# Kernel optimization log

Measured on AMD Instinct MI355X. Metric: run time of the kernel, lower is better.

The kernel has to match this reference:

```python
import jax, jax.numpy as jnp
import numpy as np

B, DIM, H, W = 8, 512, 32, 32
NUM_HEADS, KEY_DIM, VALUE_DIM, DIM_OUT = 8, 64, 64, 512


def setup_inputs() -> dict:
    key = jax.random.key(0)
    ks = jax.random.split(key, 5)
    return {
        "x": jax.random.normal(ks[0], (B, DIM, H, W), dtype=jnp.float32),
        "query_proj": jax.random.normal(ks[1], (NUM_HEADS, KEY_DIM, DIM), dtype=jnp.float32),
        "key_proj": jax.random.normal(ks[2], (DIM, KEY_DIM), dtype=jnp.float32),
        "value_proj": jax.random.normal(ks[3], (DIM, VALUE_DIM), dtype=jnp.float32),
        "out_proj": jax.random.normal(ks[4], (DIM_OUT, NUM_HEADS, VALUE_DIM), dtype=jnp.float32),
    }


def reference(x, query_proj, key_proj, value_proj, out_proj):
    b, d, h, w = x.shape
    key_dim = query_proj.shape[1]
    scale = key_dim ** (-0.5)
    # flatten spatial dims to tokens: [b, n, d] where n = h*w (m == x here)
    rx = jnp.transpose(x.reshape(b, d, h * w), (0, 2, 1))
    q = jnp.einsum('bnd,hkd->bnhk', rx, query_proj)
    k = jnp.einsum('bmd,dk->bmk', rx, key_proj)          # single shared K head
    attn = jax.nn.softmax(jnp.einsum('bnhk,bmk->bnhm', q, k) * scale, axis=-1)
    v = jnp.einsum('bmd,dv->bmv', rx, value_proj)        # single shared V head
    o = jnp.einsum('bnhm,bmv->bnhv', attn, v)
    result = jnp.einsum('bnhv,dhv->bdn', o, out_proj)
    return result.reshape(b, -1, h, w)
```

## Files before the change

kernel.cpp:

```cpp
#include <hip/hip_runtime.h>
#include <math.h>

#define BATCH 8
#define DIMD  512
#define NTOK  1024
#define NH    8
#define CQKV  640
#define DOUT  512

typedef __attribute__((ext_vector_type(8))) short short8;
typedef __attribute__((ext_vector_type(4))) short short4v;
typedef __attribute__((ext_vector_type(4))) float f32x4;

__device__ __forceinline__ short bf16rn(float x) {
    unsigned u = __float_as_uint(x);
    u += 0x7FFF + ((u >> 16) & 1);
    return (short)(u >> 16);
}
__device__ __forceinline__ float bf16tof(short s) {
    return __uint_as_float(((unsigned)(unsigned short)s) << 16);
}
struct HL { short h, l; };
__device__ __forceinline__ HL bf16split(float x) {
    HL r;
    r.h = bf16rn(x);
    r.l = bf16rn(x - bf16tof(r.h));
    return r;
}
__device__ __forceinline__ void dma16(const short* g, short* l) {
    __builtin_amdgcn_global_load_lds(
        (const __attribute__((address_space(1))) unsigned int*)g,
        (__attribute__((address_space(3))) unsigned int*)l, 16, 0, 0);
}
__device__ __forceinline__ float swzmax16(float v) {
    v = fmaxf(v, __int_as_float(__builtin_amdgcn_ds_swizzle(__float_as_int(v), 0x041F)));
    v = fmaxf(v, __int_as_float(__builtin_amdgcn_ds_swizzle(__float_as_int(v), 0x081F)));
    v = fmaxf(v, __int_as_float(__builtin_amdgcn_ds_swizzle(__float_as_int(v), 0x101F)));
    v = fmaxf(v, __int_as_float(__builtin_amdgcn_ds_swizzle(__float_as_int(v), 0x201F)));
    return v;
}
__device__ __forceinline__ unsigned packbf2(float f0, float f1) {
    return __builtin_amdgcn_perm(__float_as_uint(f1), __float_as_uint(f0), 0x07060302);
}


__global__ __launch_bounds__(256) void prepack_all(const float* __restrict__ x,
                                                   const float* __restrict__ qp,
                                                   const float* __restrict__ kp,
                                                   const float* __restrict__ vp,
                                                   const float* __restrict__ wout,
                                                   short* __restrict__ whi,
                                                   short* __restrict__ wlo,
                                                   short* __restrict__ xhi,
                                                   short* __restrict__ xlo,
                                                   short* __restrict__ wof) {
    __shared__ float Cs[64][65];
    const int blk = blockIdx.x;
    const int t = threadIdx.x;
    if (blk < 1024) {
        const int nt = blk & 15, dt = (blk >> 4) & 7, b = blk >> 7;
        #pragma unroll
        for (int i = 0; i < 4; ++i) {
            int row = (t >> 4) + i * 16;
            float4 v = *(const float4*)(x + ((size_t)(b * DIMD + dt * 64 + row)) * NTOK
                                          + nt * 64 + (t & 15) * 4);
            Cs[row][(t & 15) * 4 + 0] = v.x;
            Cs[row][(t & 15) * 4 + 1] = v.y;
            Cs[row][(t & 15) * 4 + 2] = v.z;
            Cs[row][(t & 15) * 4 + 3] = v.w;
        }
        __syncthreads();
        for (int u = t; u < 512; u += 256) {
            int lane2 = u & 63, cidx = u >> 6;
            int q2 = lane2 >> 4, r2 = lane2 & 15;
            int kt_loc = cidx & 1, mt_loc = cidx >> 1;
            short8 h8, l8;
            #pragma unroll
            for (int j = 0; j < 8; ++j) {
                HL s = bf16split(Cs[kt_loc * 32 + q2 * 8 + j][mt_loc * 16 + r2]);
                h8[j] = s.h; l8[j] = s.l;
            }
            size_t off = (((size_t)(b * 64 + nt * 4 + mt_loc)) * 16 + dt * 2 + kt_loc) * 512
                         + lane2 * 8;
            *(short8*)&xhi[off] = h8;
            *(short8*)&xlo[off] = l8;
        }
    } else if (blk < 1184) {
        int tid = (blk - 1024) * 256 + t;
        int lane = tid & 63, kt = (tid >> 6) & 15, ct = tid >> 10;
        int q = lane >> 4, r = lane & 15;
        int c = ct * 16 + r;
        short8 h, l;
        #pragma unroll
        for (int j = 0; j < 8; ++j) {
            int d = kt * 32 + q * 8 + j;
            float v;
            if (c < 64)       v = kp[d * 64 + c];
            else if (c < 128) v = vp[d * 64 + (c - 64)];
            else              v = qp[(size_t)(c - 128) * DIMD + d];
            HL s = bf16split(v);
            h[j] = s.h; l[j] = s.l;
        }
        *(short8*)&whi[(size_t)tid * 8] = h;
        *(short8*)&wlo[(size_t)tid * 8] = l;
    } else {
        int tid = (blk - 1184) * 256 + t;
        int lane = tid & 63, kt = (tid >> 6) & 15, mt = tid >> 10;
        int q = lane >> 4, r = lane & 15;
        const float* src = wout + (size_t)(mt * 16 + r) * DOUT + kt * 32 + q * 8;
        short8 h;
        #pragma unroll
        for (int j = 0; j < 8; ++j) h[j] = bf16rn(src[j]);
        *(short8*)&wof[(size_t)tid * 8] = h;
    }
}

__global__ __launch_bounds__(256) void qkv_gemm(const short* __restrict__ xhi,
                                                const short* __restrict__ xlo,
                                                const short* __restrict__ whi,
                                                const short* __restrict__ wlo,
                                                short* __restrict__ khi,
                                                short* __restrict__ klo,
                                                short* __restrict__ vf,
                                                short* __restrict__ qhi,
                                                short* __restrict__ qlo) {
    __shared__ __align__(16) char pool[49152];
    short* Ah = (short*)pool;
    short* Al = Ah + 8192;
    short* Bh = Al + 8192;
    short* Bl = Bh + 4096;
    float (*Cs)[65] = (float(*)[65])pool;

    const int idx = blockIdx.x;
    const int low = idx & 7, rest = idx >> 3;
    const int cb = rest % 10, gh = rest / 10;
    const int g = gh * 8 + low;
    const int b = g >> 3, bml = g & 7;

    const int tid = threadIdx.x, w = tid >> 6, lane = tid & 63;
    const int q = lane >> 4, r = lane & 15;
    f32x4 acc[2][4];
    #pragma unroll
    for (int i = 0; i < 2; ++i)
        #pragma unroll
        for (int j = 0; j < 4; ++j) acc[i][j] = (f32x4){0.f, 0.f, 0.f, 0.f};

    for (int it = 0; it < 8; ++it) {
        __syncthreads();
        for (int u = w; u < 16; u += 4) {
            size_t ga = ((size_t)((b * 64 + bml * 8 + (u >> 1)) * 16 + it * 2 + (u & 1))) * 512 + lane * 8;
            dma16(xhi + ga, &Ah[u * 512]);
            dma16(xlo + ga, &Al[u * 512]);
            if (u < 8) {
                size_t gb = ((size_t)((cb * 4 + (u >> 1)) * 16 + it * 2 + (u & 1))) * 512 + lane * 8;
                dma16(whi + gb, &Bh[u * 512]);
                dma16(wlo + gb, &Bl[u * 512]);
            }
        }
        __syncthreads();
        #pragma unroll
        for (int kc = 0; kc < 2; ++kc) {
            short8 ah[2], al[2];
            #pragma unroll
            for (int rt = 0; rt < 2; ++rt) {
                ah[rt] = *(short8*)&Ah[((w * 2 + rt) * 2 + kc) * 512 + lane * 8];
                al[rt] = *(short8*)&Al[((w * 2 + rt) * 2 + kc) * 512 + lane * 8];
            }
            #pragma unroll
            for (int tt = 0; tt < 4; ++tt) {
                short8 bh = *(short8*)&Bh[(tt * 2 + kc) * 512 + lane * 8];
                short8 bl = *(short8*)&Bl[(tt * 2 + kc) * 512 + lane * 8];
                #pragma unroll
                for (int rt = 0; rt < 2; ++rt) {
                    acc[rt][tt] = __builtin_amdgcn_mfma_f32_16x16x32_bf16(ah[rt], bh, acc[rt][tt], 0, 0, 0);
                    acc[rt][tt] = __builtin_amdgcn_mfma_f32_16x16x32_bf16(ah[rt], bl, acc[rt][tt], 0, 0, 0);
                    acc[rt][tt] = __builtin_amdgcn_mfma_f32_16x16x32_bf16(al[rt], bh, acc[rt][tt], 0, 0, 0);
                }
            }
        }
    }

    __syncthreads();
    #pragma unroll
    for (int rt = 0; rt < 2; ++rt)
        #pragma unroll
        for (int reg = 0; reg < 4; ++reg)
            #pragma unroll
            for (int tt = 0; tt < 4; ++tt)
                Cs[w * 32 + rt * 16 + q * 4 + reg][tt * 16 + r] = acc[rt][tt][reg];
    __syncthreads();

    if (cb == 0) {
        for (int u = tid; u < 1024; u += 256) {
            int lane2 = u & 63, ic = (u >> 6) & 7, tl = u >> 9;
            int q2 = lane2 >> 4, r2 = lane2 & 15;
            int i = ic >> 1, cc = ic & 1;
            short8 h8, l8;
            #pragma unroll
            for (int j = 0; j < 8; ++j) {
                HL s = bf16split(Cs[tl * 64 + i * 16 + r2][cc * 32 + q2 * 8 + j]);
                h8[j] = s.h; l8[j] = s.l;
            }
            size_t off = ((size_t)(b * 16 + bml * 2 + tl) * 8 + ic) * 512 + lane2 * 8;
            *(short8*)&khi[off] = h8;
            *(short8*)&klo[off] = l8;
        }
    } else if (cb == 1) {
        for (int u = tid; u < 1024; u += 256) {
            int lane2 = u & 63, ic = (u >> 6) & 7, tl = u >> 9;
            int q2 = lane2 >> 4, r2 = lane2 & 15;
            int tv = ic >> 1, cc = ic & 1;
            short8 v8;
            #pragma unroll
            for (int j = 0; j < 8; ++j)
                v8[j] = bf16rn(Cs[tl * 64 + cc * 32 + q2 * 8 + j][tv * 16 + r2]);
            size_t off = ((size_t)(b * 16 + bml * 2 + tl) * 8 + ic) * 512 + lane2 * 8;
            *(short8*)&vf[off] = v8;
        }
    } else {
        const int hd = cb - 2;
        const float qscale = 0.125f * 1.44269504f;
        for (int u = tid; u < 1024; u += 256) {
            int lane2 = u & 63, ch = u >> 6;
            int q2 = lane2 >> 4, r2 = lane2 & 15;
            int kc = ch & 1, ntl = ch >> 1;
            short8 h8, l8;
            #pragma unroll
            for (int j = 0; j < 8; ++j) {
                HL s = bf16split(Cs[ntl * 16 + r2][kc * 32 + q2 * 8 + j] * qscale);
                h8[j] = s.h; l8[j] = s.l;
            }
            size_t off = ((((size_t)(b * 8 + hd) * 64 + bml * 8 + ntl) * 2 + kc) * 64 + lane2) * 8;
            *(short8*)&qhi[off] = h8;
            *(short8*)&qlo[off] = l8;
        }
    }
}

__global__ __launch_bounds__(512) void attn_mfma(const short* __restrict__ qhi_g,
                                                 const short* __restrict__ qlo_g,
                                                 const short* __restrict__ khi_g,
                                                 const short* __restrict__ klo_g,
                                                 const short* __restrict__ vf_g,
                                                 short* __restrict__ ob) {
    __shared__ short Khi[2][4096], Klo[2][4096], Vf[2][4096];
    __shared__ short Pbuf[8 * 64 * 20];
    const int blk = blockIdx.x;
    const int b   = blk & 7;
    const int h   = (blk >> 3) & 7;
    const int qt  = blk >> 6;
    const int tid = threadIdx.x;
    const int w    = tid >> 6;
    const int lane = tid & 63;
    const int q    = lane >> 4;
    const int r    = lane & 15;
    short* Pw = Pbuf + w * (64 * 20);
    const int nt = qt * 8 + w;

    short8 qhi[2], qlo[2];
    #pragma unroll
    for (int c = 0; c < 2; ++c) {
        size_t off = ((((size_t)(b * 8 + h) * 64 + nt) * 2 + c) * 64 + lane) * 8;
        qhi[c] = *(const short8*)&qhi_g[off];
        qlo[c] = *(const short8*)&qlo_g[off];
    }

    short8 bones;
    #pragma unroll
    for (int j = 0; j < 8; ++j) bones[j] = (short)0x3F80;

    f32x4 oacc[4], lacc;
    float m_[4];
    #pragma unroll
    for (int tt = 0; tt < 4; ++tt) oacc[tt] = (f32x4){0.f, 0.f, 0.f, 0.f};
    lacc = (f32x4){0.f, 0.f, 0.f, 0.f};
    #pragma unroll
    for (int i = 0; i < 4; ++i) m_[i] = -1e30f;

    {
        const size_t kb = ((size_t)(b * 16 + 0) * 8) * 512;
        dma16(khi_g + kb + w * 512 + lane * 8, &Khi[0][w * 512]);
        dma16(klo_g + kb + w * 512 + lane * 8, &Klo[0][w * 512]);
        dma16(vf_g  + kb + w * 512 + lane * 8, &Vf [0][w * 512]);
    }

    for (int t = 0; t < 16; ++t) {
        const int cur = t & 1;
        __builtin_amdgcn_sched_barrier(0);
        asm volatile("s_waitcnt vmcnt(0) lgkmcnt(0)" ::: "memory");
        __builtin_amdgcn_sched_barrier(0);
        __syncthreads();
        if (t < 15) {
            const size_t kb = ((size_t)(b * 16 + t + 1) * 8) * 512;
            dma16(khi_g + kb + w * 512 + lane * 8, &Khi[cur ^ 1][w * 512]);
            dma16(klo_g + kb + w * 512 + lane * 8, &Klo[cur ^ 1][w * 512]);
            dma16(vf_g  + kb + w * 512 + lane * 8, &Vf [cur ^ 1][w * 512]);
        }

        f32x4 s[4];
        #pragma unroll
        for (int tt = 0; tt < 4; ++tt) s[tt] = (f32x4){0.f, 0.f, 0.f, 0.f};
        #pragma unroll
        for (int c = 0; c < 2; ++c) {
            #pragma unroll
            for (int tt = 0; tt < 4; ++tt) {
                short8 kh = *(short8*)&Khi[cur][((tt * 2 + c) * 64 + lane) * 8];
                short8 kl = *(short8*)&Klo[cur][((tt * 2 + c) * 64 + lane) * 8];
                s[tt] = __builtin_amdgcn_mfma_f32_16x16x32_bf16(qhi[c], kh, s[tt], 0, 0, 0);
                s[tt] = __builtin_amdgcn_mfma_f32_16x16x32_bf16(qhi[c], kl, s[tt], 0, 0, 0);
                s[tt] = __builtin_amdgcn_mfma_f32_16x16x32_bf16(qlo[c], kh, s[tt], 0, 0, 0);
            }
        }

        float pmax[4];
        bool need = false;
        #pragma unroll
        for (int reg = 0; reg < 4; ++reg) {
            float pm = fmaxf(fmaxf(s[0][reg], s[1][reg]), fmaxf(s[2][reg], s[3][reg]));
            pmax[reg] = pm;
            need = need || (pm > m_[reg] + 30.f);
        }
        if (__any((int)need)) {
            #pragma unroll
            for (int reg = 0; reg < 4; ++reg) {
                float smax = swzmax16(pmax[reg]);
                float nm    = fmaxf(m_[reg], smax);
                float alpha = exp2f(m_[reg] - nm);
                m_[reg] = nm;
                lacc[reg] *= alpha;
                #pragma unroll
                for (int tt = 0; tt < 4; ++tt) oacc[tt][reg] *= alpha;
            }
        }
        #pragma unroll
        for (int reg = 0; reg < 4; ++reg)
            #pragma unroll
            for (int tt = 0; tt < 4; ++tt)
                s[tt][reg] = exp2f(s[tt][reg] - m_[reg]);

        #pragma unroll
        for (int tt = 0; tt < 4; ++tt) {
            uint2 pk;
            pk.x = packbf2(s[tt][0], s[tt][1]);
            pk.y = packbf2(s[tt][2], s[tt][3]);
            *(uint2*)&Pw[(r + 16 * tt) * 20 + q * 4] = pk;
        }

        #pragma unroll
        for (int c = 0; c < 2; ++c) {
            short8 pf;
            #pragma unroll
            for (int j = 0; j < 8; ++j)
                pf[j] = Pw[(c * 32 + q * 8 + j) * 20 + r];
            lacc = __builtin_amdgcn_mfma_f32_16x16x32_bf16(pf, bones, lacc, 0, 0, 0);
            #pragma unroll
            for (int tt = 0; tt < 4; ++tt) {
                short8 vfr = *(short8*)&Vf[cur][((tt * 2 + c) * 64 + lane) * 8];
                oacc[tt] = __builtin_amdgcn_mfma_f32_16x16x32_bf16(pf, vfr, oacc[tt], 0, 0, 0);
            }
        }
    }

    #pragma unroll
    for (int reg = 0; reg < 4; ++reg) {
        float inv = 1.f / lacc[reg];
        #pragma unroll
        for (int tt = 0; tt < 4; ++tt) {
            int ct = h * 2 + (tt >> 1);
            int lanep = ((tt & 1) * 2 + (r >> 3)) * 16 + q * 4 + reg;
            ob[((((size_t)b * 64 + nt) * 16 + ct) * 64 + lanep) * 8 + (r & 7)] =
                bf16rn(oacc[tt][reg] * inv);
        }
    }
}

__global__ __launch_bounds__(256) void out_gemm(const short* __restrict__ wof,
                                                const short* __restrict__ obf,
                                                float* __restrict__ out) {
    __shared__ short Ah[2][4096];
    __shared__ short Bh[2][4096];
    const int b = blockIdx.z, bd = blockIdx.y, bn = blockIdx.x;
    const int tid = threadIdx.x, w = tid >> 6, lane = tid & 63;
    const int q = lane >> 4, r = lane & 15;
    f32x4 acc[4];
    #pragma unroll
    for (int j = 0; j < 4; ++j) acc[j] = (f32x4){0.f, 0.f, 0.f, 0.f};

    for (int u = w; u < 8; u += 4) {
        size_t ga = ((size_t)((bd * 4 + (u >> 1)) * 16 + (u & 1))) * 512 + lane * 8;
        dma16(wof + ga, &Ah[0][u * 512]);
        size_t gb = ((size_t)((b * 64 + bn * 4 + (u >> 1)) * 16 + (u & 1))) * 512 + lane * 8;
        dma16(obf + gb, &Bh[0][u * 512]);
    }

    for (int it = 0; it < 8; ++it) {
        const int cur = it & 1;
        __syncthreads();
        if (it < 7) {
            for (int u = w; u < 8; u += 4) {
                size_t ga = ((size_t)((bd * 4 + (u >> 1)) * 16 + (it + 1) * 2 + (u & 1))) * 512 + lane * 8;
                dma16(wof + ga, &Ah[cur ^ 1][u * 512]);
                size_t gb = ((size_t)((b * 64 + bn * 4 + (u >> 1)) * 16 + (it + 1) * 2 + (u & 1))) * 512 + lane * 8;
                dma16(obf + gb, &Bh[cur ^ 1][u * 512]);
            }
        }
        #pragma unroll
        for (int kc = 0; kc < 2; ++kc) {
            short8 a = *(short8*)&Ah[cur][(w * 2 + kc) * 512 + lane * 8];
            #pragma unroll
            for (int tt = 0; tt < 4; ++tt) {
                short8 bb = *(short8*)&Bh[cur][(tt * 2 + kc) * 512 + lane * 8];
                acc[tt] = __builtin_amdgcn_mfma_f32_16x16x32_bf16(a, bb, acc[tt], 0, 0, 0);
            }
        }
    }
    const int d_base = bd * 64 + w * 16;
    #pragma unroll
    for (int reg = 0; reg < 4; ++reg)
        #pragma unroll
        for (int tt = 0; tt < 4; ++tt)
            out[((size_t)b * DOUT + d_base + q * 4 + reg) * NTOK
                + bn * 64 + tt * 16 + r] = acc[tt][reg];
}

extern "C" void kernel_launch(void* const* d_in, const int* in_sizes, int n_in,
                              void* d_out, int out_size, void* d_ws, size_t ws_size,
                              hipStream_t stream) {
    const float* x  = (const float*)d_in[0];
    const float* qp = (const float*)d_in[1];
    const float* kp = (const float*)d_in[2];
    const float* vp = (const float*)d_in[3];
    const float* op = (const float*)d_in[4];
    float* out = (float*)d_out;

    short* Whi = (short*)d_ws;
    short* Wlo = Whi + 327680;
    short* Xhi = Wlo + 327680;
    short* Xlo = Xhi + 4194304;
    short* Qhi = Xlo + 4194304;
    short* Qlo = Qhi + 4194304;
    short* Khi = Qlo + 4194304;
    short* Klo = Khi + 524288;
    short* Vf  = Klo + 524288;
    short* Wof = Vf  + 524288;
    short* Ob  = Xhi;

    prepack_all <<<1312, 256, 0, stream>>>(x, qp, kp, vp, op,
                                           Whi, Wlo, Xhi, Xlo, Wof);
    qkv_gemm    <<<640, 256, 0, stream>>>(Xhi, Xlo, Whi, Wlo,
                                          Khi, Klo, Vf, Qhi, Qlo);
    attn_mfma   <<<512, 512, 0, stream>>>(Qhi, Qlo, Khi, Klo, Vf, Ob);
    out_gemm    <<<dim3(16, 8, BATCH), 256, 0, stream>>>(Wof, Ob, out);
}
```

Baseline: 158.3 us.

## Compute transposed scores to feed P directly into PV MFMA without LDS

The QK^T MFMA operands are swapped so the score tile comes out transposed. Its bf16-packed accumulator registers can then serve directly as the A operand of 16x16x16 MFMAs for the P·V and row-sum products. This removes the per-wave LDS P buffer with its scattered element reads, and replaces the swizzle-based row max with a per-lane max plus two xor shuffles and a broadcast of alpha. The cost is twice as many smaller MFMAs for PV and a different V fragment indexing, with an inline-asm fallback when the builtin is unavailable.

Result: no change. 155.4 us (-1.8%).

```diff
diff --git a/kernel.cpp b/kernel.cpp
--- a/kernel.cpp
+++ b/kernel.cpp
@@ -32,16 +32,30 @@
         (const __attribute__((address_space(1))) unsigned int*)g,
         (__attribute__((address_space(3))) unsigned int*)l, 16, 0, 0);
 }
-__device__ __forceinline__ float swzmax16(float v) {
-    v = fmaxf(v, __int_as_float(__builtin_amdgcn_ds_swizzle(__float_as_int(v), 0x041F)));
-    v = fmaxf(v, __int_as_float(__builtin_amdgcn_ds_swizzle(__float_as_int(v), 0x081F)));
-    v = fmaxf(v, __int_as_float(__builtin_amdgcn_ds_swizzle(__float_as_int(v), 0x101F)));
-    v = fmaxf(v, __int_as_float(__builtin_amdgcn_ds_swizzle(__float_as_int(v), 0x201F)));
-    return v;
-}
 __device__ __forceinline__ unsigned packbf2(float f0, float f1) {
     return __builtin_amdgcn_perm(__float_as_uint(f1), __float_as_uint(f0), 0x07060302);
 }
+
+#if defined(__has_builtin)
+#if __has_builtin(__builtin_amdgcn_mfma_f32_16x16x16bf16_1k)
+#define HAVE_MFMA16_BUILTIN 1
+__device__ __forceinline__ f32x4 mfma16(short4v a, short4v b, f32x4 c) {
+    return __builtin_amdgcn_mfma_f32_16x16x16bf16_1k(a, b, c, 0, 0, 0);
+}
+#elif __has_builtin(__builtin_amdgcn_mfma_f32_16x16x16_bf16)
+#define HAVE_MFMA16_BUILTIN 1
+__device__ __forceinline__ f32x4 mfma16(short4v a, short4v b, f32x4 c) {
+    return __builtin_amdgcn_mfma_f32_16x16x16_bf16(a, b, c, 0, 0, 0);
+}
+#endif
+#endif
+#ifndef HAVE_MFMA16_BUILTIN
+__device__ __forceinline__ f32x4 mfma16(short4v a, short4v b, f32x4 c) {
+    asm("s_nop 1\n\tv_mfma_f32_16x16x16_bf16 %0, %1, %2, %0"
+        : "+v"(c) : "v"(a), "v"(b));
+    return c;
+}
+#endif
 
 
 __global__ __launch_bounds__(256) void prepack_all(const float* __restrict__ x,
@@ -244,7 +258,6 @@
                                                  const short* __restrict__ vf_g,
                                                  short* __restrict__ ob) {
     __shared__ short Khi[2][4096], Klo[2][4096], Vf[2][4096];
-    __shared__ short Pbuf[8 * 64 * 20];
     const int blk = blockIdx.x;
     const int b   = blk & 7;
     const int h   = (blk >> 3) & 7;
@@ -254,7 +267,6 @@
     const int lane = tid & 63;
     const int q    = lane >> 4;
     const int r    = lane & 15;
-    short* Pw = Pbuf + w * (64 * 20);
     const int nt = qt * 8 + w;
 
     short8 qhi[2], qlo[2];
@@ -265,17 +277,18 @@
         qlo[c] = *(const short8*)&qlo_g[off];
     }
 
-    short8 bones;
-    #pragma unroll
-    for (int j = 0; j < 8; ++j) bones[j] = (short)0x3F80;
+    short4v bones4;
+    #pragma unroll
+    for (int j = 0; j < 4; ++j) bones4[j] = (short)0x3F80;
 
     f32x4 oacc[4], lacc;
-    float m_[4];
     #pragma unroll
     for (int tt = 0; tt < 4; ++tt) oacc[tt] = (f32x4){0.f, 0.f, 0.f, 0.f};
     lacc = (f32x4){0.f, 0.f, 0.f, 0.f};
-    #pragma unroll
-    for (int i = 0; i < 4; ++i) m_[i] = -1e30f;
+    float m_ = -1e30f;
+
+    const int kbase = lane * 8;
+    const int vbase = ((q >> 1) * 16 + r) * 8 + (q & 1) * 4;
 
     {
         const size_t kb = ((size_t)(b * 16 + 0) * 8) * 512;
@@ -297,69 +310,67 @@
             dma16(vf_g  + kb + w * 512 + lane * 8, &Vf [cur ^ 1][w * 512]);
         }
 
-        f32x4 s[4];
-        #pragma unroll
-        for (int tt = 0; tt < 4; ++tt) s[tt] = (f32x4){0.f, 0.f, 0.f, 0.f};
-        #pragma unroll
-        for (int c = 0; c < 2; ++c) {
+        f32x4 sT[4];
+        #pragma unroll
+        for (int i = 0; i < 4; ++i) sT[i] = (f32x4){0.f, 0.f, 0.f, 0.f};
+        #pragma unroll
+        for (int cc = 0; cc < 2; ++cc) {
+            #pragma unroll
+            for (int i = 0; i < 4; ++i) {
+                short8 kh = *(short8*)&Khi[cur][(i * 2 + cc) * 512 + kbase];
+                short8 kl = *(short8*)&Klo[cur][(i * 2 + cc) * 512 + kbase];
+                sT[i] = __builtin_amdgcn_mfma_f32_16x16x32_bf16(kh, qhi[cc], sT[i], 0, 0, 0);
+                sT[i] = __builtin_amdgcn_mfma_f32_16x16x32_bf16(kl, qhi[cc], sT[i], 0, 0, 0);
+                sT[i] = __builtin_amdgcn_mfma_f32_16x16x32_bf16(kh, qlo[cc], sT[i], 0, 0, 0);
+            }
+        }
+
+        float pm;
+        {
+            float a0 = fmaxf(fmaxf(sT[0][0], sT[0][1]), fmaxf(sT[0][2], sT[0][3]));
+            float a1 = fmaxf(fmaxf(sT[1][0], sT[1][1]), fmaxf(sT[1][2], sT[1][3]));
+            float a2 = fmaxf(fmaxf(sT[2][0], sT[2][1]), fmaxf(sT[2][2], sT[2][3]));
+            float a3 = fmaxf(fmaxf(sT[3][0], sT[3][1]), fmaxf(sT[3][2], sT[3][3]));
+            pm = fmaxf(fmaxf(a0, a1), fmaxf(a2, a3));
+        }
+        bool need = (pm > m_ + 30.f);
+        if (__any((int)need)) {
+            float full = fmaxf(pm, __shfl_xor(pm, 16));
+            full = fmaxf(full, __shfl_xor(full, 32));
+            float nm = fmaxf(m_, full);
+            float alpha = exp2f(m_ - nm);
+            m_ = nm;
+            #pragma unroll
+            for (int reg = 0; reg < 4; ++reg) {
+                float areg = __shfl(alpha, q * 20 + reg);
+                lacc[reg] *= areg;
+                #pragma unroll
+                for (int tt = 0; tt < 4; ++tt) oacc[tt][reg] *= areg;
+            }
+        }
+        #pragma unroll
+        for (int i = 0; i < 4; ++i)
+            #pragma unroll
+            for (int reg = 0; reg < 4; ++reg)
+                sT[i][reg] = exp2f(sT[i][reg] - m_);
+
+        #pragma unroll
+        for (int c = 0; c < 4; ++c) {
+            union { uint2 u; short4v s; } pk;
+            pk.u.x = packbf2(sT[c][0], sT[c][1]);
+            pk.u.y = packbf2(sT[c][2], sT[c][3]);
+            short4v pf = pk.s;
+            lacc = mfma16(pf, bones4, lacc);
             #pragma unroll
             for (int tt = 0; tt < 4; ++tt) {
-                short8 kh = *(short8*)&Khi[cur][((tt * 2 + c) * 64 + lane) * 8];
-                short8 kl = *(short8*)&Klo[cur][((tt * 2 + c) * 64 + lane) * 8];
-                s[tt] = __builtin_amdgcn_mfma_f32_16x16x32_bf16(qhi[c], kh, s[tt], 0, 0, 0);
-                s[tt] = __builtin_amdgcn_mfma_f32_16x16x32_bf16(qhi[c], kl, s[tt], 0, 0, 0);
-                s[tt] = __builtin_amdgcn_mfma_f32_16x16x32_bf16(qlo[c], kh, s[tt], 0, 0, 0);
-            }
-        }
-
-        float pmax[4];
-        bool need = false;
-        #pragma unroll
-        for (int reg = 0; reg < 4; ++reg) {
-            float pm = fmaxf(fmaxf(s[0][reg], s[1][reg]), fmaxf(s[2][reg], s[3][reg]));
-            pmax[reg] = pm;
-            need = need || (pm > m_[reg] + 30.f);
-        }
-        if (__any((int)need)) {
-            #pragma unroll
-            for (int reg = 0; reg < 4; ++reg) {
-                float smax = swzmax16(pmax[reg]);
-                float nm    = fmaxf(m_[reg], smax);
-                float alpha = exp2f(m_[reg] - nm);
-                m_[reg] = nm;
-                lacc[reg] *= alpha;
-                #pragma unroll
-                for (int tt = 0; tt < 4; ++tt) oacc[tt][reg] *= alpha;
-            }
-        }
-        #pragma unroll
-        for (int reg = 0; reg < 4; ++reg)
-            #pragma unroll
-            for (int tt = 0; tt < 4; ++tt)
-                s[tt][reg] = exp2f(s[tt][reg] - m_[reg]);
-
-        #pragma unroll
-        for (int tt = 0; tt < 4; ++tt) {
-            uint2 pk;
-            pk.x = packbf2(s[tt][0], s[tt][1]);
-            pk.y = packbf2(s[tt][2], s[tt][3]);
-            *(uint2*)&Pw[(r + 16 * tt) * 20 + q * 4] = pk;
-        }
-
-        #pragma unroll
-        for (int c = 0; c < 2; ++c) {
-            short8 pf;
-            #pragma unroll
-            for (int j = 0; j < 8; ++j)
-                pf[j] = Pw[(c * 32 + q * 8 + j) * 20 + r];
-            lacc = __builtin_amdgcn_mfma_f32_16x16x32_bf16(pf, bones, lacc, 0, 0, 0);
-            #pragma unroll
-            for (int tt = 0; tt < 4; ++tt) {
-                short8 vfr = *(short8*)&Vf[cur][((tt * 2 + c) * 64 + lane) * 8];
-                oacc[tt] = __builtin_amdgcn_mfma_f32_16x16x32_bf16(pf, vfr, oacc[tt], 0, 0, 0);
-            }
-        }
-    }
+                short4v vfr = *(const short4v*)
+                    &Vf[cur][vbase + (tt * 2 + (c >> 1)) * 512 + (c & 1) * 256];
+                oacc[tt] = mfma16(pf, vfr, oacc[tt]);
+            }
+        }
+    }
+
+    asm volatile("s_nop 7\n\ts_nop 7" :::);
 
     #pragma unroll
     for (int reg = 0; reg < 4; ++reg) {
```
